# Optimization experiments

Hardware: AMD Instinct MI355X
Metric: run time of the kernel (lower is better)

The kernel has to match this reference:

```python
import jax, jax.numpy as jnp
import numpy as np

B, R, C, W, HEADS = 4, 32, 96, 4, 4
SHIFT = W // 2
N = W ** 3                      # tokens per window = 64
NW = (R // W) ** 3              # windows per sample = 512
MLP = 4 * C
EPS = 1e-5


def _build_attn_mask():
    img = np.zeros((R, R, R), dtype=np.float32)
    slices = (slice(0, -W), slice(-W, -SHIFT), slice(-SHIFT, None))
    cnt = 0
    for xs in slices:
        for ys in slices:
            for zs in slices:
                img[xs, ys, zs] = cnt
                cnt += 1
    m = img.reshape(R // W, W, R // W, W, R // W, W)
    m = m.transpose(0, 2, 4, 1, 3, 5).reshape(NW, N)          # (nW, N)
    diff = m[:, None, :] - m[:, :, None]                       # (nW, N, N)
    return np.where(diff != 0, -100.0, 0.0).astype(np.float32)


def setup_inputs() -> dict:
    key = jax.random.key(0)
    ks = jax.random.split(key, 8)
    s = 0.02
    return {
        "inputs": jax.random.normal(ks[0], (B, R ** 3, C), jnp.float32),
        "norm1_g": jnp.ones((C,), jnp.float32),
        "norm1_b": jnp.zeros((C,), jnp.float32),
        "qkv_w": jax.random.normal(ks[1], (C, 3 * C), jnp.float32) * s,
        "qkv_b": jnp.zeros((3 * C,), jnp.float32),
        "proj_w": jax.random.normal(ks[2], (C, C), jnp.float32) * s,
        "proj_b": jnp.zeros((C,), jnp.float32),
        "norm2_g": jnp.ones((C,), jnp.float32),
        "norm2_b": jnp.zeros((C,), jnp.float32),
        "mlp_w1": jax.random.normal(ks[3], (C, MLP), jnp.float32) * s,
        "mlp_b1": jnp.zeros((MLP,), jnp.float32),
        "mlp_w2": jax.random.normal(ks[4], (MLP, C), jnp.float32) * s,
        "mlp_b2": jnp.zeros((C,), jnp.float32),
        "attn_mask": jnp.asarray(_build_attn_mask()),
    }


def _layernorm(x, g, b):
    mu = jnp.mean(x, axis=-1, keepdims=True)
    var = jnp.mean(jnp.square(x - mu), axis=-1, keepdims=True)
    return (x - mu) * jax.lax.rsqrt(var + EPS) * g + b


def _box_partition(x):
    # (B, R, R, R, C) -> (B*nW, N, C)
    x = x.reshape(B, R // W, W, R // W, W, R // W, W, C)
    x = x.transpose(0, 1, 3, 5, 2, 4, 6, 7)
    return x.reshape(-1, N, C)


def _box_reverse(boxes):
    # (B*nW, N, C) -> (B, R, R, R, C)
    x = boxes.reshape(B, R // W, R // W, R // W, W, W, W, C)
    x = x.transpose(0, 1, 4, 2, 5, 3, 6, 7)
    return x.reshape(B, R, R, R, C)


def _forward(inputs, norm1_g, norm1_b, qkv_w, qkv_b, proj_w, proj_b,
             norm2_g, norm2_b, mlp_w1, mlp_b1, mlp_w2, mlp_b2, attn_mask):
    shortcut = inputs
    x = _layernorm(inputs, norm1_g, norm1_b)
    x = x.reshape(B, R, R, R, C)
    x = jnp.roll(x, shift=(-SHIFT, -SHIFT, -SHIFT), axis=(1, 2, 3))
    boxes = _box_partition(x)                                   # (B*nW, N, C)

    dh = C // HEADS
    qkv = boxes @ qkv_w + qkv_b                                 # (B*nW, N, 3C)
    qkv = qkv.reshape(-1, N, 3, HEADS, dh)
    q, k, v = qkv[:, :, 0], qkv[:, :, 1], qkv[:, :, 2]          # (B*nW, N, H, dh)
    scale = dh ** -0.5
    attn = jnp.einsum('wnhd,wmhd->whnm', q, k) * scale          # (B*nW, H, N, N)
    attn = attn.reshape(B, NW, HEADS, N, N) + attn_mask[None, :, None]
    attn = jax.nn.softmax(attn.reshape(-1, HEADS, N, N), axis=-1)
    out = jnp.einsum('whnm,wmhd->wnhd', attn, v).reshape(-1, N, C)
    out = out @ proj_w + proj_b                                 # (B*nW, N, C)

    x = _box_reverse(out)
    x = jnp.roll(x, shift=(SHIFT, SHIFT, SHIFT), axis=(1, 2, 3))
    x = x.reshape(B, R ** 3, C)
    x = x * 0.5 + shortcut                                      # drop_path=0 -> identity

    h = _layernorm(x, norm2_g, norm2_b)
    h = jax.nn.gelu(h @ mlp_w1 + mlp_b1) @ mlp_w2 + mlp_b2
    return h * 0.5 + x


def reference(inputs, norm1_g, norm1_b, qkv_w, qkv_b, proj_w, proj_b,
              norm2_g, norm2_b, mlp_w1, mlp_b1, mlp_w2, mlp_b2, attn_mask):
    return _forward(inputs, norm1_g, norm1_b, qkv_w, qkv_b, proj_w, proj_b,
                    norm2_g, norm2_b, mlp_w1, mlp_b1, mlp_w2, mlp_b2, attn_mask)
```

## Files before the change

kernel.cpp:

```cpp
#include <hip/hip_runtime.h>
#include <hip/hip_bf16.h>

#define CC 96
#define LDXP 104
#define KOFF 6656
#define XOFF 6656
#define KST 136
#define VST 72

typedef __bf16 bf16;
typedef __attribute__((ext_vector_type(8))) __bf16 bf16x8;
typedef __attribute__((ext_vector_type(4))) float f32x4;

#define MFMA16(a, b, c) __builtin_amdgcn_mfma_f32_16x16x32_bf16(a, b, c, 0, 0, 0)

__device__ __attribute__((aligned(16))) bf16 g_w1t[384 * 96];
__device__ __attribute__((aligned(16))) bf16 g_w2t[96 * 384];
__device__ __attribute__((aligned(16))) bf16 g_qkvwt[288 * 96];
__device__ __attribute__((aligned(16))) bf16 g_projwt[96 * 96];

template<bool BF>
__device__ __forceinline__ float ldg(const void* p, size_t i) {
    if constexpr (BF) return (float)((const bf16*)p)[i];
    else              return ((const float*)p)[i];
}

template<bool BF>
__device__ __forceinline__ void ld24(const void* p, size_t base, float* v) {
    if constexpr (BF) {
        const bf16* q = (const bf16*)p + base;
        #pragma unroll
        for (int i = 0; i < 3; i++) {
            bf16x8 f = *(const bf16x8*)(q + i * 8);
            #pragma unroll
            for (int j = 0; j < 8; j++) v[i * 8 + j] = (float)f[j];
        }
    } else {
        #pragma unroll
        for (int i = 0; i < 24; i++) v[i] = ((const float*)p)[base + i];
    }
}

__device__ __forceinline__ void st24_lds(bf16* dst, const float* v) {
    #pragma unroll
    for (int i = 0; i < 3; i++) {
        bf16x8 f;
        #pragma unroll
        for (int j = 0; j < 8; j++) f[j] = (bf16)v[i * 8 + j];
        *(bf16x8*)(dst + i * 8) = f;
    }
}

template<bool BF>
__device__ __forceinline__ void st24_glob(const bf16* stage, void* out, size_t g) {
    if constexpr (BF) {
        #pragma unroll
        for (int i = 0; i < 3; i++)
            *(bf16x8*)((bf16*)out + g + i * 8) = *(const bf16x8*)(stage + i * 8);
    } else {
        #pragma unroll
        for (int i = 0; i < 6; i++) {
            f32x4 v;
            #pragma unroll
            for (int j = 0; j < 4; j++) v[j] = (float)stage[i * 4 + j];
            *(f32x4*)((float*)out + g + i * 4) = v;
        }
    }
}

__device__ __forceinline__ bf16x8 ldsA(const bf16* base, int row0, int ld, int k0) {
    const int l = threadIdx.x & 63;
    return *(const bf16x8*)(base + (row0 + (l & 15)) * ld + k0 + (l >> 4) * 8);
}
__device__ __forceinline__ bf16x8 gB(const bf16* base, int n0, int K, int k0) {
    const int l = threadIdx.x & 63;
    return *(const bf16x8*)(base + (n0 + (l & 15)) * K + k0 + (l >> 4) * 8);
}

__device__ __forceinline__ float gelu_f(float x) {
    const float u = 1.5957691216057308f * (x + 0.044715f * x * x * x);
    return x - x * __builtin_amdgcn_rcpf(__expf(u) + 1.0f);
}

template<bool BF>
__device__ void tbody(int idx, const void* qkv_w, const void* proj_w,
                      const void* w1, const void* w2) {
    if (idx < 384 * 96) {
        int n = idx / 96, k = idx % 96;
        g_w1t[idx] = (bf16)ldg<BF>(w1, (size_t)k * 384 + n);
    } else if (idx < 2 * 384 * 96) {
        int j = idx - 384 * 96; int n = j / 384, k = j % 384;
        g_w2t[j] = (bf16)ldg<BF>(w2, (size_t)k * 96 + n);
    } else if (idx < 2 * 384 * 96 + 288 * 96) {
        int j = idx - 2 * 384 * 96; int n = j / 96, k = j % 96;
        g_qkvwt[j] = (bf16)ldg<BF>(qkv_w, (size_t)k * 288 + n);
    } else {
        int j = idx - 2 * 384 * 96 - 288 * 96;
        if (j < 96 * 96) {
            int n = j / 96, k = j % 96;
            g_projwt[j] = (bf16)ldg<BF>(proj_w, (size_t)k * 96 + n);
        }
    }
}
__global__ __launch_bounds__(256) void transpose_kernel(
    const void* g1, const void* qkv_w, const void* proj_w, const void* w1, const void* w2) {
    const int idx = blockIdx.x * 256 + threadIdx.x;
    if (((const unsigned*)g1)[0] == 0x3F803F80u) tbody<true >(idx, qkv_w, proj_w, w1, w2);
    else                                         tbody<false>(idx, qkv_w, proj_w, w1, w2);
}

template<bool BF>
__device__ void fused_body(const void* x_in, const void* g1v, const void* b1v,
                           const void* qkv_b, const void* proj_b,
                           const void* g2v, const void* b2v, const void* mb1,
                           const void* mb2, void* out,
                           bf16* bufA, bf16* bufX, int* src_s)
{
    const int t = threadIdx.x;
    const int w = t >> 6;
    const int l = t & 63;
    const int box = blockIdx.x;
    const int b = box >> 9, bx = (box >> 6) & 7, by = (box >> 3) & 7, bz = box & 7;
    const bool b7x = (bx == 7), b7y = (by == 7), b7z = (bz == 7);
    const bool boundary = b7x || b7y || b7z;
    auto gc = [&](int n) -> int {
        return ((b7x && (n & 32)) ? 4 : 0) | ((b7y && (n & 8)) ? 2 : 0)
             | ((b7z && (n & 2)) ? 1 : 0);
    };
    const int qkvS = w * 4 + (w < 2 ? w : 2), qkvC = 5 - (w >> 1);
    const int sixS = w + (w < 2 ? w : 2),     sixC = 2 - (w >> 1);

    {
        const int row = t >> 2, hh = t & 3;
        *(f32x4*)(bufX + KOFF + row * KST + hh * 32 + 24) = (f32x4){0.f, 0.f, 0.f, 0.f};
        if (t < 64) *(f32x4*)(bufX + t * LDXP + 96) = (f32x4){0.f, 0.f, 0.f, 0.f};
    }

    {
        const int row = t >> 2, quad = t & 3;
        const int wx = row >> 4, wy = (row >> 2) & 3, wz = row & 3;
        const int sx = (bx * 4 + wx + 2) & 31;
        const int sy = (by * 4 + wy + 2) & 31;
        const int sz = (bz * 4 + wz + 2) & 31;
        const int src = ((b * 32 + sx) * 32 + sy) * 32 + sz;
        if (quad == 0) src_s[row] = src;
        float v[24];
        ld24<BF>(x_in, (size_t)src * CC + quad * 24, v);
        float s = 0.f, ss = 0.f;
        #pragma unroll
        for (int i = 0; i < 24; i++) { s += v[i]; ss += v[i] * v[i]; }
        s += __shfl_xor(s, 1);  ss += __shfl_xor(ss, 1);
        s += __shfl_xor(s, 2);  ss += __shfl_xor(ss, 2);
        const float mu = s * (1.f / 96.f);
        const float rstd = rsqrtf(ss * (1.f / 96.f) - mu * mu + 1e-5f);
        float o[24];
        #pragma unroll
        for (int i = 0; i < 24; i++) {
            const int c = quad * 24 + i;
            o[i] = (v[i] - mu) * rstd * ldg<BF>(g1v, c) + ldg<BF>(b1v, c);
        }
        st24_lds(bufA + row * LDXP + quad * 24, o);
    }
    __syncthreads();

    {
        bf16x8 aF[12];
        #pragma unroll
        for (int qt = 0; qt < 4; qt++)
            #pragma unroll
            for (int k = 0; k < 3; k++)
                aF[qt * 3 + k] = ldsA(bufA, qt * 16, LDXP, k * 32);
        __syncthreads();

        for (int i = 0; i < qkvC; i++) {
            const int nt = qkvS + i;
            const bf16x8 bB0 = gB(g_qkvwt, nt * 16, 96, 0);
            const bf16x8 bB1 = gB(g_qkvwt, nt * 16, 96, 32);
            const bf16x8 bB2 = gB(g_qkvwt, nt * 16, 96, 64);
            const int col = nt * 16 + (l & 15);
            const float bias = ldg<BF>(qkv_b, col);
            #pragma unroll
            for (int qt = 0; qt < 4; qt++) {
                f32x4 acc = {0.f, 0.f, 0.f, 0.f};
                acc = MFMA16(aF[qt * 3 + 0], bB0, acc);
                acc = MFMA16(aF[qt * 3 + 1], bB1, acc);
                acc = MFMA16(aF[qt * 3 + 2], bB2, acc);
                const int rq = qt * 16 + ((l >> 4) << 2);
                if (nt < 6) {
                    #pragma unroll
                    for (int r = 0; r < 4; r++)
                        bufX[(rq + r) * LDXP + col] = (bf16)(acc[r] + bias);
                } else if (nt < 12) {
                    const int c = col - 96, hh = c / 24, d = c - hh * 24;
                    #pragma unroll
                    for (int r = 0; r < 4; r++)
                        bufX[KOFF + (rq + r) * KST + hh * 32 + d] = (bf16)(acc[r] + bias);
                } else {
                    const int c = col - 192;
                    #pragma unroll
                    for (int r = 0; r < 4; r++)
                        bufA[c * VST + rq + r] = (bf16)(acc[r] + bias);
                }
            }
        }
    }
    __syncthreads();

    {
        const int h = w;
        bf16x8 aQ[4], bK[4], bV[2][2];
        #pragma unroll
        for (int qt = 0; qt < 4; qt++)
            aQ[qt] = *(const bf16x8*)(bufX + (qt * 16 + (l & 15)) * LDXP + h * 24 + ((l >> 4) << 3));
        #pragma unroll
        for (int mt = 0; mt < 4; mt++)
            bK[mt] = *(const bf16x8*)(bufX + KOFF + (mt * 16 + (l & 15)) * KST + h * 32 + ((l >> 4) << 3));
        #pragma unroll
        for (int ks = 0; ks < 2; ks++)
            #pragma unroll
            for (int nt = 0; nt < 2; nt++)
                bV[ks][nt] = *(const bf16x8*)(bufA + (h * 24 + nt * 8 + (l & 15)) * VST
                                              + ks * 32 + ((l >> 4) << 3));
        __syncthreads();

        f32x4 S[4][4];
        #pragma unroll
        for (int qt = 0; qt < 4; qt++)
            #pragma unroll
            for (int mt = 0; mt < 4; mt++)
                S[qt][mt] = MFMA16(aQ[qt], bK[mt], ((f32x4){0.f, 0.f, 0.f, 0.f}));

        const float scale = 0.20412414523193154f;
        bf16* pB = bufX + h * 4096;
        int gcol[4];
        if (boundary) {
            #pragma unroll
            for (int mt = 0; mt < 4; mt++) gcol[mt] = gc(mt * 16 + (l & 15));
        }
        #pragma unroll
        for (int qt = 0; qt < 4; qt++) {
            float e[4][4], rs[4] = {0.f, 0.f, 0.f, 0.f};
            if (boundary) {
                int grow[4];
                #pragma unroll
                for (int r = 0; r < 4; r++)
                    grow[r] = gc(qt * 16 + ((l >> 4) << 2) + r);
                #pragma unroll
                for (int mt = 0; mt < 4; mt++)
                    #pragma unroll
                    for (int r = 0; r < 4; r++) {
                        float ev = __expf(S[qt][mt][r] * scale);
                        ev = (grow[r] == gcol[mt]) ? ev : 0.f;
                        e[mt][r] = ev; rs[r] += ev;
                    }
            } else {
                #pragma unroll
                for (int mt = 0; mt < 4; mt++)
                    #pragma unroll
                    for (int r = 0; r < 4; r++) {
                        const float ev = __expf(S[qt][mt][r] * scale);
                        e[mt][r] = ev; rs[r] += ev;
                    }
            }
            #pragma unroll
            for (int r = 0; r < 4; r++) {
                rs[r] += __shfl_xor(rs[r], 1);
                rs[r] += __shfl_xor(rs[r], 2);
                rs[r] += __shfl_xor(rs[r], 4);
                rs[r] += __shfl_xor(rs[r], 8);
            }
            float ri[4];
            #pragma unroll
            for (int r = 0; r < 4; r++) ri[r] = __builtin_amdgcn_rcpf(rs[r]);
            #pragma unroll
            for (int mt = 0; mt < 4; mt++) {
                const int colm = mt * 16 + (l & 15);
                const int chl = colm >> 3;
                #pragma unroll
                for (int r = 0; r < 4; r++) {
                    const int row = qt * 16 + ((l >> 4) << 2) + r;
                    const int ch = chl ^ (row & 7);
                    pB[row * 64 + ch * 8 + (colm & 7)] = (bf16)(e[mt][r] * ri[r]);
                }
            }
        }

        f32x4 O[4][2];
        #pragma unroll
        for (int qt = 0; qt < 4; qt++)
            #pragma unroll
            for (int nt = 0; nt < 2; nt++) O[qt][nt] = (f32x4){0.f, 0.f, 0.f, 0.f};
        #pragma unroll
        for (int ks = 0; ks < 2; ks++)
            #pragma unroll
            for (int qt = 0; qt < 4; qt++) {
                const int row = qt * 16 + (l & 15);
                const int ch = (ks * 4 + (l >> 4)) ^ (row & 7);
                const bf16x8 aP = *(const bf16x8*)(pB + row * 64 + ch * 8);
                O[qt][0] = MFMA16(aP, bV[ks][0], O[qt][0]);
                O[qt][1] = MFMA16(aP, bV[ks][1], O[qt][1]);
            }

        #pragma unroll
        for (int qt = 0; qt < 4; qt++)
            #pragma unroll
            for (int nt = 0; nt < 2; nt++) {
                const int cl = nt * 8 + (l & 15);
                if (nt == 0 || (l & 15) >= 8) {
                    #pragma unroll
                    for (int r = 0; r < 4; r++) {
                        const int row = qt * 16 + ((l >> 4) << 2) + r;
                        bufA[row * LDXP + h * 24 + cl] = (bf16)O[qt][nt][r];
                    }
                }
            }
    }
    __syncthreads();

    {
        bf16x8 pF[12];
        #pragma unroll
        for (int qt = 0; qt < 4; qt++)
            #pragma unroll
            for (int k = 0; k < 3; k++)
                pF[qt * 3 + k] = ldsA(bufA, qt * 16, LDXP, k * 32);
        __syncthreads();
        {
            const int row = t >> 2, quad = t & 3;
            float v[24];
            ld24<BF>(x_in, (size_t)src_s[row] * CC + quad * 24, v);
            st24_lds(bufA + row * LDXP + quad * 24, v);
        }
        __syncthreads();

        for (int i = 0; i < sixC; i++) {
            const int nt = sixS + i;
            const bf16x8 bB0 = gB(g_projwt, nt * 16, 96, 0);
            const bf16x8 bB1 = gB(g_projwt, nt * 16, 96, 32);
            const bf16x8 bB2 = gB(g_projwt, nt * 16, 96, 64);
            const int col = nt * 16 + (l & 15);
            const float bias = ldg<BF>(proj_b, col);
            #pragma unroll
            for (int qt = 0; qt < 4; qt++) {
                f32x4 acc = {0.f, 0.f, 0.f, 0.f};
                acc = MFMA16(pF[qt * 3 + 0], bB0, acc);
                acc = MFMA16(pF[qt * 3 + 1], bB1, acc);
                acc = MFMA16(pF[qt * 3 + 2], bB2, acc);
                const int rq = qt * 16 + ((l >> 4) << 2);
                #pragma unroll
                for (int r = 0; r < 4; r++) {
                    const float x2v = 0.5f * (acc[r] + bias)
                                    + (float)bufA[(rq + r) * LDXP + col];
                    bufX[XOFF + (rq + r) * LDXP + col] = (bf16)x2v;
                }
            }
        }
    }
    __syncthreads();

    {
        const int row = t >> 2, quad = t & 3;
        float v[24];
        #pragma unroll
        for (int i = 0; i < 3; i++) {
            bf16x8 f = *(const bf16x8*)(bufX + XOFF + row * LDXP + quad * 24 + i * 8);
            #pragma unroll
            for (int j = 0; j < 8; j++) v[i * 8 + j] = (float)f[j];
        }
        float s = 0.f, ss = 0.f;
        #pragma unroll
        for (int i = 0; i < 24; i++) { s += v[i]; ss += v[i] * v[i]; }
        s += __shfl_xor(s, 1);  ss += __shfl_xor(ss, 1);
        s += __shfl_xor(s, 2);  ss += __shfl_xor(ss, 2);
        const float mu = s * (1.f / 96.f);
        const float rstd = rsqrtf(ss * (1.f / 96.f) - mu * mu + 1e-5f);
        float o[24];
        #pragma unroll
        for (int i = 0; i < 24; i++) {
            const int c = quad * 24 + i;
            o[i] = (v[i] - mu) * rstd * ldg<BF>(g2v, c) + ldg<BF>(b2v, c);
        }
        st24_lds(bufX + row * LDXP + quad * 24, o);
    }
    __syncthreads();

    {
        bf16x8 mF[12];
        #pragma unroll
        for (int qt = 0; qt < 4; qt++)
            #pragma unroll
            for (int k = 0; k < 3; k++)
                mF[qt * 3 + k] = ldsA(bufX, qt * 16, LDXP, k * 32);

        f32x4 C[2][4];
        #pragma unroll
        for (int i = 0; i < 2; i++)
            #pragma unroll
            for (int qt = 0; qt < 4; qt++) C[i][qt] = (f32x4){0.f, 0.f, 0.f, 0.f};

        for (int c = 0; c < 4; c++) {
            if (c) __syncthreads();
            for (int i = 0; i < sixC; i++) {
                const int lt = sixS + i;
                const int n0 = c * 96 + lt * 16;
                const bf16x8 bB0 = gB(g_w1t, n0, 96, 0);
                const bf16x8 bB1 = gB(g_w1t, n0, 96, 32);
                const bf16x8 bB2 = gB(g_w1t, n0, 96, 64);
                const int colc = lt * 16 + (l & 15);
                const float bias = ldg<BF>(mb1, c * 96 + colc);
                #pragma unroll
                for (int qt = 0; qt < 4; qt++) {
                    f32x4 acc = {0.f, 0.f, 0.f, 0.f};
                    acc = MFMA16(mF[qt * 3 + 0], bB0, acc);
                    acc = MFMA16(mF[qt * 3 + 1], bB1, acc);
                    acc = MFMA16(mF[qt * 3 + 2], bB2, acc);
                    const int rq = qt * 16 + ((l >> 4) << 2);
                    #pragma unroll
                    for (int r = 0; r < 4; r++)
                        bufA[(rq + r) * LDXP + colc] = (bf16)gelu_f(acc[r] + bias);
                }
            }
            __syncthreads();
            bf16x8 hF[12];
            #pragma unroll
            for (int qt = 0; qt < 4; qt++) {
                hF[qt * 3 + 0] = ldsA(bufA, qt * 16, LDXP, 0);
                hF[qt * 3 + 1] = ldsA(bufA, qt * 16, LDXP, 32);
                hF[qt * 3 + 2] = ldsA(bufA, qt * 16, LDXP, 64);
            }
            for (int i = 0; i < sixC; i++) {
                const int ot = sixS + i;
                const bf16x8 bB0 = gB(g_w2t, ot * 16, 384, c * 96);
                const bf16x8 bB1 = gB(g_w2t, ot * 16, 384, c * 96 + 32);
                const bf16x8 bB2 = gB(g_w2t, ot * 16, 384, c * 96 + 64);
                #pragma unroll
                for (int qt = 0; qt < 4; qt++) {
                    C[i][qt] = MFMA16(hF[qt * 3 + 0], bB0, C[i][qt]);
                    C[i][qt] = MFMA16(hF[qt * 3 + 1], bB1, C[i][qt]);
                    C[i][qt] = MFMA16(hF[qt * 3 + 2], bB2, C[i][qt]);
                }
            }
        }
        __syncthreads();

        for (int i = 0; i < sixC; i++) {
            const int ot = sixS + i;
            const int col = ot * 16 + (l & 15);
            const float bias = ldg<BF>(mb2, col);
            #pragma unroll
            for (int qt = 0; qt < 4; qt++) {
                const int rq = qt * 16 + ((l >> 4) << 2);
                #pragma unroll
                for (int r = 0; r < 4; r++) {
                    const float res = (float)bufX[XOFF + (rq + r) * LDXP + col];
                    bufA[(rq + r) * LDXP + col] = (bf16)(0.5f * (C[i][qt][r] + bias) + res);
                }
            }
        }
        __syncthreads();
        {
            const int row = t >> 2, quad = t & 3;
            st24_glob<BF>(bufA + row * LDXP + quad * 24, out,
                          (size_t)src_s[row] * CC + quad * 24);
        }
    }
}

__global__ __launch_bounds__(256, 3) void fused_kernel(
    const void* x_in, const void* g1, const void* b1, const void* qkv_b,
    const void* proj_b, const void* g2, const void* b2,
    const void* mb1, const void* mb2, void* out) {
    __shared__ bf16 bufA[6912];
    __shared__ bf16 bufX[16384];
    __shared__ int src_s[64];
    if (((const unsigned*)g1)[0] == 0x3F803F80u)
        fused_body<true >(x_in, g1, b1, qkv_b, proj_b, g2, b2, mb1, mb2, out,
                          bufA, bufX, src_s);
    else
        fused_body<false>(x_in, g1, b1, qkv_b, proj_b, g2, b2, mb1, mb2, out,
                          bufA, bufX, src_s);
}

extern "C" void kernel_launch(void* const* d_in, const int* in_sizes, int n_in,
                              void* d_out, int out_size, void* d_ws, size_t ws_size,
                              hipStream_t stream) {
    const void* x_in   = d_in[0];
    const void* g1     = d_in[1];
    const void* b1     = d_in[2];
    const void* qkv_w  = d_in[3];
    const void* qkv_b  = d_in[4];
    const void* proj_w = d_in[5];
    const void* proj_b = d_in[6];
    const void* g2     = d_in[7];
    const void* b2     = d_in[8];
    const void* w1     = d_in[9];
    const void* bias1  = d_in[10];
    const void* w2     = d_in[11];
    const void* bias2  = d_in[12];

    transpose_kernel<<<432, 256, 0, stream>>>(g1, qkv_w, proj_w, w1, w2);
    fused_kernel<<<2048, 256, 0, stream>>>(x_in, g1, b1, qkv_b, proj_b,
                                           g2, b2, bias1, bias2, d_out);
}
```

Baseline: 213.6 us.

## Keep residual in registers, stream attention per q-tile, shrink LDS footprint

The first LayerNorm pass now stores the input row as bf16 in registers and writes it to the residual region of shared memory during attention. This removes the second global reload of the shortcut and two block barriers before the projection. The P·V step is done per 16-row query tile, so each head's probability scratch falls from 4096 to 1024 elements and total shared memory shrinks, which may allow more resident blocks. The GELU is also reformulated with an fma and a negated exponent. Risks are more register pressure from the held residual and a write into the XOFF region that must not overlap the per-head P scratch.

```diff
diff --git a/kernel.cpp b/kernel.cpp
--- a/kernel.cpp
+++ b/kernel.cpp
@@ -78,8 +78,9 @@
 }
 
 __device__ __forceinline__ float gelu_f(float x) {
-    const float u = 1.5957691216057308f * (x + 0.044715f * x * x * x);
-    return x - x * __builtin_amdgcn_rcpf(__expf(u) + 1.0f);
+    const float s = x * x;
+    const float r = x * __builtin_fmaf(0.044715f, s, 1.0f);
+    return x * __builtin_amdgcn_rcpf(1.0f + __expf(-1.5957691216057308f * r));
 }
 
 template<bool BF>
@@ -130,6 +131,8 @@
     const int qkvS = w * 4 + (w < 2 ? w : 2), qkvC = 5 - (w >> 1);
     const int sixS = w + (w < 2 ? w : 2),     sixC = 2 - (w >> 1);
 
+    bf16x8 resid[3];
+
     {
         const int row = t >> 2, hh = t & 3;
         *(f32x4*)(bufX + KOFF + row * KST + hh * 32 + 24) = (f32x4){0.f, 0.f, 0.f, 0.f};
@@ -146,6 +149,13 @@
         if (quad == 0) src_s[row] = src;
         float v[24];
         ld24<BF>(x_in, (size_t)src * CC + quad * 24, v);
+        #pragma unroll
+        for (int i = 0; i < 3; i++) {
+            bf16x8 f;
+            #pragma unroll
+            for (int j = 0; j < 8; j++) f[j] = (bf16)v[i * 8 + j];
+            resid[i] = f;
+        }
         float s = 0.f, ss = 0.f;
         #pragma unroll
         for (int i = 0; i < 24; i++) { s += v[i]; ss += v[i] * v[i]; }
@@ -230,8 +240,15 @@
             for (int mt = 0; mt < 4; mt++)
                 S[qt][mt] = MFMA16(aQ[qt], bK[mt], ((f32x4){0.f, 0.f, 0.f, 0.f}));
 
+        {
+            const int row = t >> 2, quad = t & 3;
+            #pragma unroll
+            for (int i = 0; i < 3; i++)
+                *(bf16x8*)(bufX + XOFF + row * LDXP + quad * 24 + i * 8) = resid[i];
+        }
+
         const float scale = 0.20412414523193154f;
-        bf16* pB = bufX + h * 4096;
+        bf16* pB = bufX + h * 1024;
         int gcol[4];
         if (boundary) {
             #pragma unroll
@@ -278,42 +295,33 @@
                 const int chl = colm >> 3;
                 #pragma unroll
                 for (int r = 0; r < 4; r++) {
-                    const int row = qt * 16 + ((l >> 4) << 2) + r;
-                    const int ch = chl ^ (row & 7);
-                    pB[row * 64 + ch * 8 + (colm & 7)] = (bf16)(e[mt][r] * ri[r]);
-                }
-            }
-        }
-
-        f32x4 O[4][2];
-        #pragma unroll
-        for (int qt = 0; qt < 4; qt++)
-            #pragma unroll
-            for (int nt = 0; nt < 2; nt++) O[qt][nt] = (f32x4){0.f, 0.f, 0.f, 0.f};
-        #pragma unroll
-        for (int ks = 0; ks < 2; ks++)
-            #pragma unroll
-            for (int qt = 0; qt < 4; qt++) {
-                const int row = qt * 16 + (l & 15);
-                const int ch = (ks * 4 + (l >> 4)) ^ (row & 7);
-                const bf16x8 aP = *(const bf16x8*)(pB + row * 64 + ch * 8);
-                O[qt][0] = MFMA16(aP, bV[ks][0], O[qt][0]);
-                O[qt][1] = MFMA16(aP, bV[ks][1], O[qt][1]);
-            }
-
-        #pragma unroll
-        for (int qt = 0; qt < 4; qt++)
+                    const int lr = ((l >> 4) << 2) + r;
+                    const int ch = chl ^ (lr & 7);
+                    pB[lr * 64 + ch * 8 + (colm & 7)] = (bf16)(e[mt][r] * ri[r]);
+                }
+            }
+            f32x4 Oq0 = {0.f, 0.f, 0.f, 0.f}, Oq1 = {0.f, 0.f, 0.f, 0.f};
+            #pragma unroll
+            for (int ks = 0; ks < 2; ks++) {
+                const int lr2 = l & 15;
+                const int ch = (ks * 4 + (l >> 4)) ^ (lr2 & 7);
+                const bf16x8 aP = *(const bf16x8*)(pB + lr2 * 64 + ch * 8);
+                Oq0 = MFMA16(aP, bV[ks][0], Oq0);
+                Oq1 = MFMA16(aP, bV[ks][1], Oq1);
+            }
             #pragma unroll
             for (int nt = 0; nt < 2; nt++) {
                 const int cl = nt * 8 + (l & 15);
                 if (nt == 0 || (l & 15) >= 8) {
+                    const f32x4 Ov = nt ? Oq1 : Oq0;
                     #pragma unroll
                     for (int r = 0; r < 4; r++) {
                         const int row = qt * 16 + ((l >> 4) << 2) + r;
-                        bufA[row * LDXP + h * 24 + cl] = (bf16)O[qt][nt][r];
+                        bufA[row * LDXP + h * 24 + cl] = (bf16)Ov[r];
                     }
                 }
             }
+        }
     }
     __syncthreads();
 
@@ -324,14 +332,6 @@
             #pragma unroll
             for (int k = 0; k < 3; k++)
                 pF[qt * 3 + k] = ldsA(bufA, qt * 16, LDXP, k * 32);
-        __syncthreads();
-        {
-            const int row = t >> 2, quad = t & 3;
-            float v[24];
-            ld24<BF>(x_in, (size_t)src_s[row] * CC + quad * 24, v);
-            st24_lds(bufA + row * LDXP + quad * 24, v);
-        }
-        __syncthreads();
 
         for (int i = 0; i < sixC; i++) {
             const int nt = sixS + i;
@@ -349,9 +349,9 @@
                 const int rq = qt * 16 + ((l >> 4) << 2);
                 #pragma unroll
                 for (int r = 0; r < 4; r++) {
-                    const float x2v = 0.5f * (acc[r] + bias)
-                                    + (float)bufA[(rq + r) * LDXP + col];
-                    bufX[XOFF + (rq + r) * LDXP + col] = (bf16)x2v;
+                    const int idx = XOFF + (rq + r) * LDXP + col;
+                    const float x2v = 0.5f * (acc[r] + bias) + (float)bufX[idx];
+                    bufX[idx] = (bf16)x2v;
                 }
             }
         }
@@ -471,7 +471,7 @@
     const void* proj_b, const void* g2, const void* b2,
     const void* mb1, const void* mb2, void* out) {
     __shared__ bf16 bufA[6912];
-    __shared__ bf16 bufX[16384];
+    __shared__ bf16 bufX[15360];
     __shared__ int src_s[64];
     if (((const unsigned*)g1)[0] == 0x3F803F80u)
         fused_body<true >(x_in, g1, b1, qkv_b, proj_b, g2, b2, mb1, mb2, out,
```

Result: no change. 212.9 us (-0.3%).
